# Kernel optimization log

Measured on AMD Instinct MI355X. Metric: run time of the kernel, lower is better.

The kernel has to match this reference:

```python
import jax, jax.numpy as jnp
import numpy as np
from jax import lax

B, M = 16384, 128
NUM_LAYERS, OW, OH = 22, 11, 11
MAX_VEC = np.array([9.0, 1.0, 1.0, 10.0, 3.0, 254.0, 1.0, 1.0, 235.0, 8.0, 9.0, 250.0,
                    29.0, 1.0, 1.0, 8.0, 1.0, 1.0, 6.0, 3.0, 1.0, 2.0], dtype=np.float32)


def setup_inputs() -> dict:
    key = jax.random.key(0)
    ks = jax.random.split(key, 20)
    s = 0.05
    return {
        "observations": jax.random.randint(ks[0], (B, M, 3), 0, 255, dtype=jnp.int32),
        "cnn1_w": jax.random.normal(ks[1], (64, 22, 5, 5), jnp.float32) * s,
        "cnn1_b": jnp.zeros((64,), jnp.float32),
        "cnn2_w": jax.random.normal(ks[2], (64, 64, 3, 3), jnp.float32) * s,
        "cnn2_b": jnp.zeros((64,), jnp.float32),
        "fc1_w": jax.random.normal(ks[3], (128, 64), jnp.float32) * s,
        "fc1_b": jnp.zeros((128,), jnp.float32),
        "enc_w": jax.random.normal(ks[4], (128, 128), jnp.float32) * s,
        "enc_b": jnp.zeros((128,), jnp.float32),
        "critic1_w": jax.random.normal(ks[5], (1024, 128), jnp.float32) * s,
        "critic1_b": jnp.zeros((1024,), jnp.float32),
        "value_w": jax.random.normal(ks[6], (1, 1024), jnp.float32) * s,
        "value_b": jnp.zeros((1,), jnp.float32),
        "actor1_w": jax.random.normal(ks[7], (512, 128), jnp.float32) * s,
        "actor1_b": jnp.zeros((512,), jnp.float32),
        "action_emb": jax.random.normal(ks[8], (100, 16), jnp.float32) * s,
        "head0_w": jax.random.normal(ks[9], (9, 528), jnp.float32) * s,
        "head0_b": jnp.zeros((9,), jnp.float32),
        "head1_w": jax.random.normal(ks[10], (10, 528), jnp.float32) * s,
        "head1_b": jnp.zeros((10,), jnp.float32),
    }


def _encode_scatter(observations):
    # zero-out any byte equal to 255 (matches torch in-place masking)
    tok = jnp.where(observations == 255, 0, observations)  # [B, M, 3]
    coords = tok[..., 0].astype(jnp.uint8)
    x = ((coords >> 4) & 15).astype(jnp.int32)
    y = (coords & 15).astype(jnp.int32)
    atr = tok[..., 1].astype(jnp.int32)
    val = tok[..., 2].astype(jnp.float32)
    b, m = atr.shape
    valid = (x < OW) & (y < OH) & (atr < NUM_LAYERS)
    b_idx = jnp.broadcast_to(jnp.arange(b, dtype=jnp.int32)[:, None], (b, m))
    b_idx = jnp.where(valid, b_idx, b)  # route invalid tokens out of bounds -> dropped
    box = jnp.zeros((b, NUM_LAYERS, OW, OH), jnp.float32)
    box = box.at[b_idx, atr, x, y].set(val, mode="drop")
    return box


def _forward(observations, cnn1_w, cnn1_b, cnn2_w, cnn2_b, fc1_w, fc1_b, enc_w, enc_b,
             critic1_w, critic1_b, value_w, value_b, actor1_w, actor1_b, action_emb,
             head0_w, head0_b, head1_w, head1_b):
    box = _encode_scatter(observations)
    x = box / jnp.asarray(MAX_VEC)[None, :, None, None]
    dn = ("NCHW", "OIHW", "NCHW")
    x = lax.conv_general_dilated(x, cnn1_w, (3, 3), "VALID", dimension_numbers=dn) + cnn1_b[None, :, None, None]
    x = lax.conv_general_dilated(x, cnn2_w, (1, 1), "VALID", dimension_numbers=dn) + cnn2_b[None, :, None, None]
    x = x.reshape(x.shape[0], -1)                 # [B, 64]
    x = x @ fc1_w.T + fc1_b                       # [B, 128]
    hidden = x @ enc_w.T + enc_b                  # [B, 128]
    critic = jnp.tanh(hidden @ critic1_w.T + critic1_b)
    value = critic @ value_w.T + value_b          # [B, 1]
    actor = hidden @ actor1_w.T + actor1_b        # [B, 512]
    emb = jnp.broadcast_to(action_emb.mean(axis=0)[None, :], (actor.shape[0], action_emb.shape[1]))
    comb = jnp.concatenate([actor, emb], axis=-1)  # [B, 528]
    logits = jnp.concatenate([comb @ head0_w.T + head0_b, comb @ head1_w.T + head1_b], axis=-1)
    return logits, value


def reference(observations, cnn1_w, cnn1_b, cnn2_w, cnn2_b, fc1_w, fc1_b, enc_w, enc_b,
              critic1_w, critic1_b, value_w, value_b, actor1_w, actor1_b, action_emb,
              head0_w, head0_b, head1_w, head1_b):
    return _forward(observations, cnn1_w, cnn1_b, cnn2_w, cnn2_b, fc1_w, fc1_b, enc_w, enc_b,
                    critic1_w, critic1_b, value_w, value_b, actor1_w, actor1_b, action_emb,
                    head0_w, head0_b, head1_w, head1_b)
```

## Files before the change

### kernel.cpp

```cpp
#include <hip/hip_runtime.h>
#include <math.h>

#define NB 16384
#define NTOK 128
#define NKEY 2662
#define NLOG 19
#define TB 32

typedef __attribute__((ext_vector_type(8))) short short8;
typedef __attribute__((ext_vector_type(4))) float floatx4;

__device__ __constant__ float c_maxv[22] = {
    9.f, 1.f, 1.f, 10.f, 3.f, 254.f, 1.f, 1.f, 235.f, 8.f, 9.f, 250.f,
    29.f, 1.f, 1.f, 8.f, 1.f, 1.f, 6.f, 3.f, 1.f, 2.f};

__device__ __forceinline__ unsigned short f2bf(float f) {
    unsigned u = __float_as_uint(f);
    return (unsigned short)((u + 0x7FFFu + ((u >> 16) & 1u)) >> 16);
}
__device__ __forceinline__ float tanh_fast(float x) {
    float e = __builtin_amdgcn_exp2f(x * 2.885390082f);
    return 1.f - 2.f * __builtin_amdgcn_rcpf(e + 1.f);
}

__global__ __launch_bounds__(256) void k_pre(
    const float* __restrict__ w1, const float* __restrict__ b1,
    const float* __restrict__ w2, const float* __restrict__ b2,
    const float* __restrict__ fc1w, const float* __restrict__ fc1b,
    const float* __restrict__ encw, const float* __restrict__ encb,
    const float* __restrict__ a1w, const float* __restrict__ a1b,
    const float* __restrict__ aemb,
    const float* __restrict__ h0w, const float* __restrict__ h0b,
    const float* __restrict__ h1w, const float* __restrict__ h1b,
    const float* __restrict__ c1w,
    float* __restrict__ G, float* __restrict__ E,
    float* __restrict__ beff, float* __restrict__ Wlog,
    float* __restrict__ blog, unsigned short* __restrict__ c1wb)
{
    __shared__ float s_w2[72 * 65];
    __shared__ float s_h2[64];
    __shared__ float s_t[128];
    __shared__ float s_emb[16];
    const int bid = blockIdx.x, t = threadIdx.x;
    if (bid < 666) {
        const int v = t & 63;
        const int key_u = __builtin_amdgcn_readfirstlane(bid * 4 + (t >> 6));
        const int key_c = (key_u < NKEY) ? key_u : (NKEY - 1);
        const int c = key_c / 121, rem = key_c % 121, X = rem / 11, Y = rem % 11;
        float acc = 0.f;
        for (int u0 = 0; u0 < 64; u0 += 8) {
            __syncthreads();
            #pragma unroll
            for (int r = 0; r < 18; ++r) {
                int g = t + 256 * r;
                int vg = g / 72, rg = g % 72;
                s_w2[rg * 65 + vg] = w2[vg * 576 + u0 * 9 + rg];
            }
            __syncthreads();
            #pragma unroll
            for (int ur = 0; ur < 8; ++ur) {
                const int w1base = (u0 + ur) * 550 + c * 25;
                #pragma unroll
                for (int i = 0; i < 3; ++i) {
                    int xi = X - 3 * i;
                    if (xi < 0 || xi > 4) continue;
                    #pragma unroll
                    for (int j = 0; j < 3; ++j) {
                        int yj = Y - 3 * j;
                        if (yj < 0 || yj > 4) continue;
                        acc += s_w2[(ur * 9 + i * 3 + j) * 65 + v] *
                               w1[w1base + xi * 5 + yj];
                    }
                }
            }
        }
        if (key_u < NKEY) G[key_u * 64 + v] = acc / c_maxv[c];
    } else if (bid < 698) {
        int m = (bid - 666) * 256 + t;
        int h = __builtin_amdgcn_readfirstlane(m >> 6) & 127;
        int v = t & 63;
        float acc = 0.f;
        #pragma unroll 8
        for (int p = 0; p < 128; ++p)
            acc += encw[h * 128 + p] * fc1w[p * 64 + v];
        E[v * 128 + h] = acc;
    } else if (bid == 698) {
        {
            int o = t >> 2, q = t & 3;
            const float* wp = w2 + (o * 64 + q * 16) * 9;
            float s = 0.f;
            #pragma unroll
            for (int ui = 0; ui < 16; ++ui) {
                float ws = 0.f;
                #pragma unroll
                for (int k = 0; k < 9; ++k) ws += wp[ui * 9 + k];
                s += b1[q * 16 + ui] * ws;
            }
            s += __shfl_xor(s, 1, 64);
            s += __shfl_xor(s, 2, 64);
            if (q == 0) s_h2[o] = s + b2[o];
        }
        __syncthreads();
        if (t < 128) {
            const float4* f4 = (const float4*)(fc1w + t * 64);
            float s = fc1b[t];
            #pragma unroll
            for (int vq = 0; vq < 16; ++vq) {
                float4 w = f4[vq];
                s += w.x * s_h2[vq * 4]     + w.y * s_h2[vq * 4 + 1] +
                     w.z * s_h2[vq * 4 + 2] + w.w * s_h2[vq * 4 + 3];
            }
            s_t[t] = s;
        } else if (t < 192) {
            int lane = t & 63;
            int e = lane & 15, rq = lane >> 4;
            float s = 0.f;
            #pragma unroll
            for (int rr = 0; rr < 25; ++rr) s += aemb[(rq * 25 + rr) * 16 + e];
            s += __shfl_xor(s, 16, 64);
            s += __shfl_xor(s, 32, 64);
            if (lane < 16) s_emb[e] = s * 0.01f;
        }
        __syncthreads();
        if (t < 128) {
            const float4* e4 = (const float4*)(encw + t * 128);
            float s = encb[t];
            #pragma unroll
            for (int pq = 0; pq < 32; ++pq) {
                float4 w = e4[pq];
                s += w.x * s_t[pq * 4]     + w.y * s_t[pq * 4 + 1] +
                     w.z * s_t[pq * 4 + 2] + w.w * s_t[pq * 4 + 3];
            }
            beff[t] = s;
        } else {
            int tp = t - 128;
            int os = tp >> 3, ai = tp & 7;
            #pragma unroll
            for (int rep = 0; rep < 2; ++rep) {
                int o = os + rep * 16;
                int oc = (o < NLOG) ? o : (NLOG - 1);
                const float* hw = (oc < 9) ? (h0w + oc * 528)
                                           : (h1w + (oc - 9) * 528);
                float s = 0.f;
                for (int a = ai; a < 528; a += 8) {
                    float m = (a < 512) ? a1b[a] : s_emb[a - 512];
                    s += hw[a] * m;
                }
                s += __shfl_xor(s, 1, 64);
                s += __shfl_xor(s, 2, 64);
                s += __shfl_xor(s, 4, 64);
                if (ai == 0 && o < NLOG)
                    blog[o] = s + ((o < 9) ? h0b[o] : h1b[o - 9]);
            }
        }
    } else if (bid < 709) {
        int n = (bid - 699) * 256 + t;
        if (n < NLOG * 128) {
            int o = __builtin_amdgcn_readfirstlane(n >> 7);
            int h = n & 127;
            const float* hw = (o < 9) ? (h0w + o * 528) : (h1w + (o - 9) * 528);
            float acc = 0.f;
            #pragma unroll 8
            for (int a = 0; a < 512; ++a)
                acc += hw[a] * a1w[a * 128 + h];
            Wlog[n] = acc;
        }
    } else {
        int n = ((bid - 709) * 256 + t) * 8;
        float4 a = *(const float4*)(c1w + n);
        float4 b4 = *(const float4*)(c1w + n + 4);
        short8 r;
        r[0] = (short)f2bf(a.x);  r[1] = (short)f2bf(a.y);
        r[2] = (short)f2bf(a.z);  r[3] = (short)f2bf(a.w);
        r[4] = (short)f2bf(b4.x); r[5] = (short)f2bf(b4.y);
        r[6] = (short)f2bf(b4.z); r[7] = (short)f2bf(b4.w);
        *(short8*)(c1wb + n) = r;
    }
}

__global__ __launch_bounds__(512, 4) void k_main(
    const int* __restrict__ obs,
    const float* __restrict__ G, const float* __restrict__ E,
    const float* __restrict__ beff,
    const unsigned short* __restrict__ c1wb, const float* __restrict__ c1b,
    const float* __restrict__ vw, const float* __restrict__ vb,
    const float* __restrict__ Wlog, const float* __restrict__ blog,
    float* __restrict__ out)
{
    __shared__ int            s_lst[TB * 32];
    __shared__ float          s_hidden[TB * 128];
    __shared__ unsigned short s_hb[TB * 136];
    __shared__ float          s_x[TB * 64];
    __shared__ float          s_E[8192];
    __shared__ int            s_cnt[TB];
    __shared__ float          s_val[8 * 32];

    const int tid = threadIdx.x, bid = blockIdx.x;
    const int b0 = bid * TB;

    const float4* E4g = (const float4*)E;
    float4 e0 = E4g[tid], e1 = E4g[tid + 512],
           e2 = E4g[tid + 1024], e3 = E4g[tid + 1536];

    if (tid < TB) s_cnt[tid] = 0;
    __syncthreads();

    {
        const int gtok0 = b0 * NTOK;
        #pragma unroll
        for (int k = 0; k < TB * NTOK / (512 * 4); ++k) {
            int g = tid + 512 * k;
            const int4* p = (const int4*)(obs + (size_t)(gtok0 + 4 * g) * 3);
            int4 A = p[0], Bv = p[1], Cv = p[2];
            int d[12] = {A.x, A.y, A.z, A.w, Bv.x, Bv.y, Bv.z, Bv.w,
                         Cv.x, Cv.y, Cv.z, Cv.w};
            #pragma unroll
            for (int s = 0; s < 4; ++s) {
                int o0 = d[3 * s], o1 = d[3 * s + 1], o2 = d[3 * s + 2];
                o0 = (o0 == 255) ? 0 : o0;
                o1 = (o1 == 255) ? 0 : o1;
                o2 = (o2 == 255) ? 0 : o2;
                int x = (o0 >> 4) & 15, y = o0 & 15;
                if (x < 11 && y < 11 && o1 < 22) {
                    int tt = 4 * g + s;
                    int bb = tt >> 7, m = tt & 127;
                    int pos = atomicAdd(&s_cnt[bb], 1);
                    if (pos < 32)
                        s_lst[bb * 32 + pos] =
                            (m << 20) | (o2 << 12) | (o1 * 121 + x * 11 + y);
                }
            }
        }
        float4* sE4 = (float4*)s_E;
        sE4[tid] = e0; sE4[tid + 512] = e1;
        sE4[tid + 1024] = e2; sE4[tid + 1536] = e3;
    }
    __syncthreads();

    {
        int bb = tid >> 4, e0i = tid & 15;
        int n = s_cnt[bb]; if (n > 32) n = 32;
        #pragma unroll
        for (int r = 0; r < 2; ++r) {
            int e = e0i + 16 * r;
            if (e < n) {
                int p = s_lst[bb * 32 + e];
                bool dead = false;
                for (int i = 0; i < n; ++i) {
                    int q = s_lst[bb * 32 + i];
                    dead |= (((q ^ p) & 0xFFF) == 0) && (q > p);
                }
                if (dead) s_lst[bb * 32 + e] = p & ~0x000FF000;
            }
        }
    }
    __syncthreads();

    {
        int w = tid >> 6, lane = tid & 63;
        #pragma unroll
        for (int jp = 0; jp < 2; ++jp) {
            int bbA = w * 4 + jp * 2, bbB = bbA + 1;
            int nA = s_cnt[bbA]; if (nA > 32) nA = 32;
            int nB = s_cnt[bbB]; if (nB > 32) nB = 32;
            int nm = (nA > nB) ? nA : nB;
            float aA = 0.f, aB = 0.f;
            for (int i = 0; i < nm; ++i) {
                if (i < nA) {
                    int p = s_lst[bbA * 32 + i];
                    aA += (float)((p >> 12) & 0xFF) * G[(p & 0xFFF) * 64 + lane];
                }
                if (i < nB) {
                    int p = s_lst[bbB * 32 + i];
                    aB += (float)((p >> 12) & 0xFF) * G[(p & 0xFFF) * 64 + lane];
                }
            }
            s_x[bbA * 64 + lane] = aA;
            s_x[bbB * 64 + lane] = aB;
        }
    }
    __syncthreads();

    {
        int g = tid >> 7, h = tid & 127;
        float be = beff[h];
        float acc[8];
        #pragma unroll
        for (int b = 0; b < 8; ++b) acc[b] = be;
        const float4* x4 = (const float4*)s_x;
        #pragma unroll
        for (int vq = 0; vq < 16; ++vq) {
            float ev0 = s_E[(vq * 4 + 0) * 128 + h];
            float ev1 = s_E[(vq * 4 + 1) * 128 + h];
            float ev2 = s_E[(vq * 4 + 2) * 128 + h];
            float ev3 = s_E[(vq * 4 + 3) * 128 + h];
            #pragma unroll
            for (int b = 0; b < 8; ++b) {
                float4 xv = x4[(g * 8 + b) * 16 + vq];
                acc[b] += xv.x * ev0 + xv.y * ev1 + xv.z * ev2 + xv.w * ev3;
            }
        }
        #pragma unroll
        for (int b = 0; b < 8; ++b) {
            int bb = g * 8 + b;
            s_hidden[bb * 128 + h] = acc[b];
            s_hb[bb * 136 + h] = f2bf(acc[b]);
        }
    }
    __syncthreads();

    {
        const int lane = tid & 63, w = tid >> 6;
        const int lm = lane & 15, quad = lane >> 4;
        short8 af0[4], af1[4];
        #pragma unroll
        for (int kk = 0; kk < 4; ++kk) {
            af0[kk] = *(const short8*)&s_hb[lm * 136 + kk * 32 + quad * 8];
            af1[kk] = *(const short8*)&s_hb[(16 + lm) * 136 + kk * 32 + quad * 8];
        }
        float vp0[4] = {0.f, 0.f, 0.f, 0.f}, vp1[4] = {0.f, 0.f, 0.f, 0.f};
        for (int nt = 0; nt < 8; ++nt) {
            int j = w * 128 + nt * 16 + lm;
            const short8* cp = (const short8*)&c1wb[j * 128];
            floatx4 a0 = {0.f, 0.f, 0.f, 0.f}, a1 = {0.f, 0.f, 0.f, 0.f};
            #pragma unroll
            for (int kk = 0; kk < 4; ++kk) {
                short8 bf = cp[kk * 4 + quad];
                a0 = __builtin_amdgcn_mfma_f32_16x16x32_bf16(af0[kk], bf, a0, 0, 0, 0);
                a1 = __builtin_amdgcn_mfma_f32_16x16x32_bf16(af1[kk], bf, a1, 0, 0, 0);
            }
            float bj = c1b[j], wj = vw[j];
            #pragma unroll
            for (int r = 0; r < 4; ++r) {
                vp0[r] += tanh_fast(a0[r] + bj) * wj;
                vp1[r] += tanh_fast(a1[r] + bj) * wj;
            }
        }
        #pragma unroll
        for (int off = 1; off <= 8; off <<= 1) {
            #pragma unroll
            for (int r = 0; r < 4; ++r) {
                vp0[r] += __shfl_xor(vp0[r], off, 64);
                vp1[r] += __shfl_xor(vp1[r], off, 64);
            }
        }
        if (lm == 0) {
            #pragma unroll
            for (int r = 0; r < 4; ++r) {
                s_val[w * 32 + quad * 4 + r]      = vp0[r];
                s_val[w * 32 + 16 + quad * 4 + r] = vp1[r];
            }
        }
    }

    {
        const float4* s_h4 = (const float4*)s_hidden;
        const float4* wl4  = (const float4*)Wlog;
        int bl = tid >> 4, oo = tid & 15;
        #pragma unroll
        for (int rep = 0; rep < 2; ++rep) {
            int o = oo + rep * 16;
            if (o < NLOG) {
                float acc = blog[o];
                #pragma unroll
                for (int hq = 0; hq < 32; ++hq) {
                    float4 hv = s_h4[bl * 32 + hq];
                    float4 wl = wl4[o * 32 + hq];
                    acc += wl.x * hv.x + wl.y * hv.y + wl.z * hv.z + wl.w * hv.w;
                }
                out[(b0 + bl) * NLOG + o] = acc;
            }
        }
    }
    __syncthreads();
    if (tid < TB) {
        float v = 0.f;
        #pragma unroll
        for (int w = 0; w < 8; ++w) v += s_val[w * 32 + tid];
        out[NB * NLOG + b0 + tid] = v + vb[0];
    }
}

extern "C" void kernel_launch(void* const* d_in, const int* in_sizes, int n_in,
                              void* d_out, int out_size, void* d_ws, size_t ws_size,
                              hipStream_t stream)
{
    const int*   obs  = (const int*)  d_in[0];
    const float* w1   = (const float*)d_in[1];
    const float* b1   = (const float*)d_in[2];
    const float* w2   = (const float*)d_in[3];
    const float* b2   = (const float*)d_in[4];
    const float* fc1w = (const float*)d_in[5];
    const float* fc1b = (const float*)d_in[6];
    const float* encw = (const float*)d_in[7];
    const float* encb = (const float*)d_in[8];
    const float* c1w  = (const float*)d_in[9];
    const float* c1b  = (const float*)d_in[10];
    const float* vw   = (const float*)d_in[11];
    const float* vb   = (const float*)d_in[12];
    const float* a1w  = (const float*)d_in[13];
    const float* a1b  = (const float*)d_in[14];
    const float* aemb = (const float*)d_in[15];
    const float* h0w  = (const float*)d_in[16];
    const float* h0b  = (const float*)d_in[17];
    const float* h1w  = (const float*)d_in[18];
    const float* h1b  = (const float*)d_in[19];

    float* W    = (float*)d_ws;
    float* G    = W;
    float* E    = W + 170368;
    float* beff = W + 178560;
    float* Wlog = W + 178688;
    float* blog = W + 181120;
    unsigned short* c1wb = (unsigned short*)(W + 181152);

    hipLaunchKernelGGL(k_pre, dim3(773), dim3(256), 0, stream,
                       w1, b1, w2, b2, fc1w, fc1b, encw, encb, a1w, a1b, aemb,
                       h0w, h0b, h1w, h1b, c1w,
                       G, E, beff, Wlog, blog, c1wb);
    hipLaunchKernelGGL(k_main, dim3(NB / TB), dim3(512), 0, stream,
                       obs, G, E, beff, c1wb, c1b, vw, vb, Wlog, blog,
                       (float*)d_out);
}
```

Measured before the change: 188.8 us.

## Halve per-block batch tile and read encoder weights from global instead of LDS

```diff
diff --git a/kernel.cpp b/kernel.cpp
--- a/kernel.cpp
+++ b/kernel.cpp
@@ -5,7 +5,7 @@
 #define NTOK 128
 #define NKEY 2662
 #define NLOG 19
-#define TB 32
+#define TB 16
 
 typedef __attribute__((ext_vector_type(8))) short short8;
 typedef __attribute__((ext_vector_type(4))) float floatx4;
@@ -178,7 +178,7 @@
     }
 }
 
-__global__ __launch_bounds__(512, 4) void k_main(
+__global__ __launch_bounds__(512, 8) void k_main(
     const int* __restrict__ obs,
     const float* __restrict__ G, const float* __restrict__ E,
     const float* __restrict__ beff,
@@ -191,118 +191,96 @@
     __shared__ float          s_hidden[TB * 128];
     __shared__ unsigned short s_hb[TB * 136];
     __shared__ float          s_x[TB * 64];
-    __shared__ float          s_E[8192];
     __shared__ int            s_cnt[TB];
-    __shared__ float          s_val[8 * 32];
+    __shared__ float          s_val[8 * 16];
 
     const int tid = threadIdx.x, bid = blockIdx.x;
     const int b0 = bid * TB;
 
-    const float4* E4g = (const float4*)E;
-    float4 e0 = E4g[tid], e1 = E4g[tid + 512],
-           e2 = E4g[tid + 1024], e3 = E4g[tid + 1536];
-
     if (tid < TB) s_cnt[tid] = 0;
     __syncthreads();
 
     {
-        const int gtok0 = b0 * NTOK;
-        #pragma unroll
-        for (int k = 0; k < TB * NTOK / (512 * 4); ++k) {
-            int g = tid + 512 * k;
-            const int4* p = (const int4*)(obs + (size_t)(gtok0 + 4 * g) * 3);
-            int4 A = p[0], Bv = p[1], Cv = p[2];
-            int d[12] = {A.x, A.y, A.z, A.w, Bv.x, Bv.y, Bv.z, Bv.w,
-                         Cv.x, Cv.y, Cv.z, Cv.w};
-            #pragma unroll
-            for (int s = 0; s < 4; ++s) {
-                int o0 = d[3 * s], o1 = d[3 * s + 1], o2 = d[3 * s + 2];
-                o0 = (o0 == 255) ? 0 : o0;
-                o1 = (o1 == 255) ? 0 : o1;
-                o2 = (o2 == 255) ? 0 : o2;
-                int x = (o0 >> 4) & 15, y = o0 & 15;
-                if (x < 11 && y < 11 && o1 < 22) {
-                    int tt = 4 * g + s;
-                    int bb = tt >> 7, m = tt & 127;
-                    int pos = atomicAdd(&s_cnt[bb], 1);
-                    if (pos < 32)
-                        s_lst[bb * 32 + pos] =
-                            (m << 20) | (o2 << 12) | (o1 * 121 + x * 11 + y);
-                }
-            }
-        }
-        float4* sE4 = (float4*)s_E;
-        sE4[tid] = e0; sE4[tid + 512] = e1;
-        sE4[tid + 1024] = e2; sE4[tid + 1536] = e3;
-    }
-    __syncthreads();
-
-    {
-        int bb = tid >> 4, e0i = tid & 15;
+        const int4* p = (const int4*)(obs + (size_t)(b0 * NTOK + 4 * tid) * 3);
+        int4 A = p[0], Bv = p[1], Cv = p[2];
+        int d[12] = {A.x, A.y, A.z, A.w, Bv.x, Bv.y, Bv.z, Bv.w,
+                     Cv.x, Cv.y, Cv.z, Cv.w};
+        #pragma unroll
+        for (int s = 0; s < 4; ++s) {
+            int o0 = d[3 * s], o1 = d[3 * s + 1], o2 = d[3 * s + 2];
+            o0 = (o0 == 255) ? 0 : o0;
+            o1 = (o1 == 255) ? 0 : o1;
+            o2 = (o2 == 255) ? 0 : o2;
+            int x = (o0 >> 4) & 15, y = o0 & 15;
+            if (x < 11 && y < 11 && o1 < 22) {
+                int tt = 4 * tid + s;
+                int bb = tt >> 7, m = tt & 127;
+                int pos = atomicAdd(&s_cnt[bb], 1);
+                if (pos < 32)
+                    s_lst[bb * 32 + pos] =
+                        (m << 20) | (o2 << 12) | (o1 * 121 + x * 11 + y);
+            }
+        }
+    }
+    __syncthreads();
+
+    {
+        int bb = tid >> 5, e = tid & 31;
         int n = s_cnt[bb]; if (n > 32) n = 32;
-        #pragma unroll
-        for (int r = 0; r < 2; ++r) {
-            int e = e0i + 16 * r;
-            if (e < n) {
-                int p = s_lst[bb * 32 + e];
-                bool dead = false;
-                for (int i = 0; i < n; ++i) {
-                    int q = s_lst[bb * 32 + i];
-                    dead |= (((q ^ p) & 0xFFF) == 0) && (q > p);
-                }
-                if (dead) s_lst[bb * 32 + e] = p & ~0x000FF000;
-            }
+        if (e < n) {
+            int p = s_lst[bb * 32 + e];
+            bool dead = false;
+            for (int i = 0; i < n; ++i) {
+                int q = s_lst[bb * 32 + i];
+                dead |= (((q ^ p) & 0xFFF) == 0) && (q > p);
+            }
+            if (dead) s_lst[bb * 32 + e] = p & ~0x000FF000;
         }
     }
     __syncthreads();
 
     {
         int w = tid >> 6, lane = tid & 63;
-        #pragma unroll
-        for (int jp = 0; jp < 2; ++jp) {
-            int bbA = w * 4 + jp * 2, bbB = bbA + 1;
-            int nA = s_cnt[bbA]; if (nA > 32) nA = 32;
-            int nB = s_cnt[bbB]; if (nB > 32) nB = 32;
-            int nm = (nA > nB) ? nA : nB;
-            float aA = 0.f, aB = 0.f;
-            for (int i = 0; i < nm; ++i) {
-                if (i < nA) {
-                    int p = s_lst[bbA * 32 + i];
-                    aA += (float)((p >> 12) & 0xFF) * G[(p & 0xFFF) * 64 + lane];
-                }
-                if (i < nB) {
-                    int p = s_lst[bbB * 32 + i];
-                    aB += (float)((p >> 12) & 0xFF) * G[(p & 0xFFF) * 64 + lane];
-                }
-            }
-            s_x[bbA * 64 + lane] = aA;
-            s_x[bbB * 64 + lane] = aB;
-        }
+        int bbA = 2 * w, bbB = 2 * w + 1;
+        int nA = s_cnt[bbA]; if (nA > 32) nA = 32;
+        int nB = s_cnt[bbB]; if (nB > 32) nB = 32;
+        int nm = (nA > nB) ? nA : nB;
+        float aA = 0.f, aB = 0.f;
+        for (int i = 0; i < nm; ++i) {
+            if (i < nA) {
+                int p = s_lst[bbA * 32 + i];
+                aA += (float)((p >> 12) & 0xFF) * G[(p & 0xFFF) * 64 + lane];
+            }
+            if (i < nB) {
+                int p = s_lst[bbB * 32 + i];
+                aB += (float)((p >> 12) & 0xFF) * G[(p & 0xFFF) * 64 + lane];
+            }
+        }
+        s_x[bbA * 64 + lane] = aA;
+        s_x[bbB * 64 + lane] = aB;
     }
     __syncthreads();
 
     {
         int g = tid >> 7, h = tid & 127;
         float be = beff[h];
-        float acc[8];
-        #pragma unroll
-        for (int b = 0; b < 8; ++b) acc[b] = be;
+        float acc[4] = {be, be, be, be};
         const float4* x4 = (const float4*)s_x;
         #pragma unroll
         for (int vq = 0; vq < 16; ++vq) {
-            float ev0 = s_E[(vq * 4 + 0) * 128 + h];
-            float ev1 = s_E[(vq * 4 + 1) * 128 + h];
-            float ev2 = s_E[(vq * 4 + 2) * 128 + h];
-            float ev3 = s_E[(vq * 4 + 3) * 128 + h];
-            #pragma unroll
-            for (int b = 0; b < 8; ++b) {
-                float4 xv = x4[(g * 8 + b) * 16 + vq];
+            float ev0 = E[(vq * 4 + 0) * 128 + h];
+            float ev1 = E[(vq * 4 + 1) * 128 + h];
+            float ev2 = E[(vq * 4 + 2) * 128 + h];
+            float ev3 = E[(vq * 4 + 3) * 128 + h];
+            #pragma unroll
+            for (int b = 0; b < 4; ++b) {
+                float4 xv = x4[(g * 4 + b) * 16 + vq];
                 acc[b] += xv.x * ev0 + xv.y * ev1 + xv.z * ev2 + xv.w * ev3;
             }
         }
         #pragma unroll
-        for (int b = 0; b < 8; ++b) {
-            int bb = g * 8 + b;
+        for (int b = 0; b < 4; ++b) {
+            int bb = g * 4 + b;
             s_hidden[bb * 128 + h] = acc[b];
             s_hb[bb * 136 + h] = f2bf(acc[b]);
         }
@@ -312,71 +290,57 @@
     {
         const int lane = tid & 63, w = tid >> 6;
         const int lm = lane & 15, quad = lane >> 4;
-        short8 af0[4], af1[4];
-        #pragma unroll
-        for (int kk = 0; kk < 4; ++kk) {
-            af0[kk] = *(const short8*)&s_hb[lm * 136 + kk * 32 + quad * 8];
-            af1[kk] = *(const short8*)&s_hb[(16 + lm) * 136 + kk * 32 + quad * 8];
-        }
-        float vp0[4] = {0.f, 0.f, 0.f, 0.f}, vp1[4] = {0.f, 0.f, 0.f, 0.f};
+        short8 af[4];
+        #pragma unroll
+        for (int kk = 0; kk < 4; ++kk)
+            af[kk] = *(const short8*)&s_hb[lm * 136 + kk * 32 + quad * 8];
+        float vp[4] = {0.f, 0.f, 0.f, 0.f};
         for (int nt = 0; nt < 8; ++nt) {
             int j = w * 128 + nt * 16 + lm;
             const short8* cp = (const short8*)&c1wb[j * 128];
-            floatx4 a0 = {0.f, 0.f, 0.f, 0.f}, a1 = {0.f, 0.f, 0.f, 0.f};
+            floatx4 a0 = {0.f, 0.f, 0.f, 0.f};
             #pragma unroll
             for (int kk = 0; kk < 4; ++kk) {
                 short8 bf = cp[kk * 4 + quad];
-                a0 = __builtin_amdgcn_mfma_f32_16x16x32_bf16(af0[kk], bf, a0, 0, 0, 0);
-                a1 = __builtin_amdgcn_mfma_f32_16x16x32_bf16(af1[kk], bf, a1, 0, 0, 0);
+                a0 = __builtin_amdgcn_mfma_f32_16x16x32_bf16(af[kk], bf, a0, 0, 0, 0);
             }
             float bj = c1b[j], wj = vw[j];
             #pragma unroll
-            for (int r = 0; r < 4; ++r) {
-                vp0[r] += tanh_fast(a0[r] + bj) * wj;
-                vp1[r] += tanh_fast(a1[r] + bj) * wj;
-            }
-        }
-        #pragma unroll
-        for (int off = 1; off <= 8; off <<= 1) {
-            #pragma unroll
-            for (int r = 0; r < 4; ++r) {
-                vp0[r] += __shfl_xor(vp0[r], off, 64);
-                vp1[r] += __shfl_xor(vp1[r], off, 64);
-            }
-        }
+            for (int r = 0; r < 4; ++r)
+                vp[r] += tanh_fast(a0[r] + bj) * wj;
+        }
+        #pragma unroll
+        for (int off = 1; off <= 8; off <<= 1)
+            #pragma unroll
+            for (int r = 0; r < 4; ++r)
+                vp[r] += __shfl_xor(vp[r], off, 64);
         if (lm == 0) {
             #pragma unroll
-            for (int r = 0; r < 4; ++r) {
-                s_val[w * 32 + quad * 4 + r]      = vp0[r];
-                s_val[w * 32 + 16 + quad * 4 + r] = vp1[r];
-            }
+            for (int r = 0; r < 4; ++r)
+                s_val[w * 16 + quad * 4 + r] = vp[r];
         }
     }
 
     {
         const float4* s_h4 = (const float4*)s_hidden;
         const float4* wl4  = (const float4*)Wlog;
-        int bl = tid >> 4, oo = tid & 15;
-        #pragma unroll
-        for (int rep = 0; rep < 2; ++rep) {
-            int o = oo + rep * 16;
-            if (o < NLOG) {
-                float acc = blog[o];
-                #pragma unroll
-                for (int hq = 0; hq < 32; ++hq) {
-                    float4 hv = s_h4[bl * 32 + hq];
-                    float4 wl = wl4[o * 32 + hq];
-                    acc += wl.x * hv.x + wl.y * hv.y + wl.z * hv.z + wl.w * hv.w;
-                }
-                out[(b0 + bl) * NLOG + o] = acc;
-            }
+        int bl = tid >> 5, o = tid & 31;
+        if (o < NLOG) {
+            float acc = blog[o];
+            #pragma unroll
+            for (int hq = 0; hq < 32; ++hq) {
+                float4 hv = s_h4[bl * 32 + hq];
+                float4 wl = wl4[o * 32 + hq];
+                acc += wl.x * hv.x + wl.y * hv.y + wl.z * hv.z + wl.w * hv.w;
+            }
+            out[(b0 + bl) * NLOG + o] = acc;
         }
     }
     __syncthreads();
     if (tid < TB) {
         float v = 0.f;
         #pragma unroll
-        for (int w = 0; w < 8; ++w) v += s_val[w * 32 + tid];
+        for (int w = 0; w < 8; ++w) v += s_val[w * 16 + tid];
         out[NB * NLOG + b0 + tid] = v + vb[0];
     }
 }
```

New measurement: 207.8 us. 1.1x slower.

## Make dedup, gather and encoder stages wave-local to drop block barriers

Applied to the files above, without the earlier changes.

```diff
diff --git a/kernel.cpp b/kernel.cpp
--- a/kernel.cpp
+++ b/kernel.cpp
@@ -238,73 +238,83 @@
     __syncthreads();
 
     {
-        int bb = tid >> 4, e0i = tid & 15;
-        int n = s_cnt[bb]; if (n > 32) n = 32;
-        #pragma unroll
-        for (int r = 0; r < 2; ++r) {
-            int e = e0i + 16 * r;
-            if (e < n) {
-                int p = s_lst[bb * 32 + e];
-                bool dead = false;
-                for (int i = 0; i < n; ++i) {
-                    int q = s_lst[bb * 32 + i];
-                    dead |= (((q ^ p) & 0xFFF) == 0) && (q > p);
-                }
-                if (dead) s_lst[bb * 32 + e] = p & ~0x000FF000;
-            }
-        }
-    }
-    __syncthreads();
-
-    {
-        int w = tid >> 6, lane = tid & 63;
-        #pragma unroll
-        for (int jp = 0; jp < 2; ++jp) {
-            int bbA = w * 4 + jp * 2, bbB = bbA + 1;
-            int nA = s_cnt[bbA]; if (nA > 32) nA = 32;
-            int nB = s_cnt[bbB]; if (nB > 32) nB = 32;
-            int nm = (nA > nB) ? nA : nB;
-            float aA = 0.f, aB = 0.f;
+        const int w = tid >> 6, lane = tid & 63;
+
+        {
+            int bb = (w << 2) + ((lane >> 4) & 3);
+            int n = s_cnt[bb]; if (n > 32) n = 32;
+            int e0i = lane & 15;
+            #pragma unroll
+            for (int r = 0; r < 2; ++r) {
+                int e = e0i + 16 * r;
+                if (e < n) {
+                    int p = s_lst[bb * 32 + e];
+                    bool dead = false;
+                    for (int i = 0; i < n; ++i) {
+                        int q = s_lst[bb * 32 + i];
+                        dead |= (((q ^ p) & 0xFFF) == 0) && (q > p);
+                    }
+                    if (dead) s_lst[bb * 32 + e] = p & ~0x000FF000;
+                }
+            }
+        }
+
+        {
+            int n4[4]; int nm = 0;
+            #pragma unroll
+            for (int q = 0; q < 4; ++q) {
+                int n = s_cnt[w * 4 + q]; if (n > 32) n = 32;
+                n4[q] = n; nm = (n > nm) ? n : nm;
+            }
+            float a4[4] = {0.f, 0.f, 0.f, 0.f};
             for (int i = 0; i < nm; ++i) {
-                if (i < nA) {
-                    int p = s_lst[bbA * 32 + i];
-                    aA += (float)((p >> 12) & 0xFF) * G[(p & 0xFFF) * 64 + lane];
-                }
-                if (i < nB) {
-                    int p = s_lst[bbB * 32 + i];
-                    aB += (float)((p >> 12) & 0xFF) * G[(p & 0xFFF) * 64 + lane];
-                }
-            }
-            s_x[bbA * 64 + lane] = aA;
-            s_x[bbB * 64 + lane] = aB;
-        }
-    }
-    __syncthreads();
-
-    {
-        int g = tid >> 7, h = tid & 127;
-        float be = beff[h];
-        float acc[8];
-        #pragma unroll
-        for (int b = 0; b < 8; ++b) acc[b] = be;
-        const float4* x4 = (const float4*)s_x;
-        #pragma unroll
-        for (int vq = 0; vq < 16; ++vq) {
-            float ev0 = s_E[(vq * 4 + 0) * 128 + h];
-            float ev1 = s_E[(vq * 4 + 1) * 128 + h];
-            float ev2 = s_E[(vq * 4 + 2) * 128 + h];
-            float ev3 = s_E[(vq * 4 + 3) * 128 + h];
-            #pragma unroll
-            for (int b = 0; b < 8; ++b) {
-                float4 xv = x4[(g * 8 + b) * 16 + vq];
-                acc[b] += xv.x * ev0 + xv.y * ev1 + xv.z * ev2 + xv.w * ev3;
-            }
-        }
-        #pragma unroll
-        for (int b = 0; b < 8; ++b) {
-            int bb = g * 8 + b;
-            s_hidden[bb * 128 + h] = acc[b];
-            s_hb[bb * 136 + h] = f2bf(acc[b]);
+                #pragma unroll
+                for (int q = 0; q < 4; ++q) {
+                    if (i < n4[q]) {
+                        int p = s_lst[(w * 4 + q) * 32 + i];
+                        a4[q] += (float)((p >> 12) & 0xFF) *
+                                 G[(p & 0xFFF) * 64 + lane];
+                    }
+                }
+            }
+            #pragma unroll
+            for (int q = 0; q < 4; ++q)
+                s_x[(w * 4 + q) * 64 + lane] = a4[q];
+        }
+
+        {
+            float be0 = beff[lane], be1 = beff[lane + 64];
+            float acc[4][2];
+            #pragma unroll
+            for (int b = 0; b < 4; ++b) { acc[b][0] = be0; acc[b][1] = be1; }
+            const float4* x4 = (const float4*)s_x;
+            #pragma unroll
+            for (int vq = 0; vq < 16; ++vq) {
+                float4 xv[4];
+                #pragma unroll
+                for (int b = 0; b < 4; ++b)
+                    xv[b] = x4[(w * 4 + b) * 16 + vq];
+                #pragma unroll
+                for (int r = 0; r < 4; ++r) {
+                    int v = vq * 4 + r;
+                    float ev0 = s_E[v * 128 + lane];
+                    float ev1 = s_E[v * 128 + lane + 64];
+                    #pragma unroll
+                    for (int b = 0; b < 4; ++b) {
+                        float xs = ((const float*)&xv[b])[r];
+                        acc[b][0] += xs * ev0;
+                        acc[b][1] += xs * ev1;
+                    }
+                }
+            }
+            #pragma unroll
+            for (int b = 0; b < 4; ++b) {
+                int bb = w * 4 + b;
+                s_hidden[bb * 128 + lane]      = acc[b][0];
+                s_hidden[bb * 128 + lane + 64] = acc[b][1];
+                s_hb[bb * 136 + lane]          = f2bf(acc[b][0]);
+                s_hb[bb * 136 + lane + 64]     = f2bf(acc[b][1]);
+            }
         }
     }
     __syncthreads();
@@ -357,20 +367,20 @@
         const float4* s_h4 = (const float4*)s_hidden;
         const float4* wl4  = (const float4*)Wlog;
         int bl = tid >> 4, oo = tid & 15;
+        float acc0 = blog[oo];
+        float acc1 = (oo < NLOG - 16) ? blog[oo + 16] : 0.f;
         #pragma unroll
-        for (int rep = 0; rep < 2; ++rep) {
-            int o = oo + rep * 16;
-            if (o < NLOG) {
-                float acc = blog[o];
-                #pragma unroll
-                for (int hq = 0; hq < 32; ++hq) {
-                    float4 hv = s_h4[bl * 32 + hq];
-                    float4 wl = wl4[o * 32 + hq];
-                    acc += wl.x * hv.x + wl.y * hv.y + wl.z * hv.z + wl.w * hv.w;
-                }
-                out[(b0 + bl) * NLOG + o] = acc;
-            }
-        }
+        for (int hq = 0; hq < 32; ++hq) {
+            float4 hv = s_h4[bl * 32 + hq];
+            float4 w0 = wl4[oo * 32 + hq];
+            acc0 += w0.x * hv.x + w0.y * hv.y + w0.z * hv.z + w0.w * hv.w;
+            if (oo < NLOG - 16) {
+                float4 w1 = wl4[(oo + 16) * 32 + hq];
+                acc1 += w1.x * hv.x + w1.y * hv.y + w1.z * hv.z + w1.w * hv.w;
+            }
+        }
+        out[(b0 + bl) * NLOG + oo] = acc0;
+        if (oo < NLOG - 16) out[(b0 + bl) * NLOG + oo + 16] = acc1;
     }
     __syncthreads();
     if (tid < TB) {
```

Result: slower. 216.3 us (+14.6%).
